# Kernel optimization log

Hardware: AMD Instinct MI355X
Metric: run time of the kernel (lower is better)

The kernel has to match this reference:

```python
import jax, jax.numpy as jnp
import numpy as np

TOP_K = 8
N_EXPERTS = 64
ALPHA = 0.1
NORM_TOPK = True
SEQ_AUX = True


def setup_inputs() -> dict:
    key = jax.random.key(0)
    k1, k2 = jax.random.split(key)
    B, S, H = 4, 4096, 2048
    hidden_states = jax.random.normal(k1, (B, S, H), dtype=jnp.float32)
    # kaiming_uniform_(a=sqrt(5)) => bound = 1/sqrt(fan_in)
    bound = 1.0 / np.sqrt(H)
    weight = jax.random.uniform(k2, (N_EXPERTS, H), dtype=jnp.float32,
                                minval=-bound, maxval=bound)
    return {"hidden_states": hidden_states, "weight": weight}


def reference(hidden_states, weight):
    B, S, H = hidden_states.shape
    E, K = N_EXPERTS, TOP_K
    x = hidden_states.reshape(-1, H)                 # [T, H], T = B*S
    logits = jnp.einsum('th,eh->te', x, weight)      # gating GEMM
    scores = jax.nn.softmax(logits, axis=-1)         # [T, E]
    topk_weight, topk_idx = jax.lax.top_k(scores, K) # [T, K]
    if K > 1 and NORM_TOPK:
        topk_weight = topk_weight / (topk_weight.sum(-1, keepdims=True) + 1e-20)

    # batch-level load stats (bincount over selections)
    expert_loads = jnp.zeros((E,), jnp.float32).at[topk_idx.reshape(-1)].add(1.0)

    # sequence-level auxiliary load-balancing loss
    if SEQ_AUX:
        idx_b = topk_idx.reshape(B, S * K)           # [B, S*K]
        ce = jnp.zeros((B, E), jnp.float32)
        ce = ce.at[jnp.arange(B)[:, None], idx_b].add(1.0)
        ce = ce / (S * K / E)
        mean_scores = scores.reshape(B, S, E).mean(axis=1)   # [B, E]
        aux_loss = (ce * mean_scores).sum(axis=1).mean() * ALPHA
    else:
        ce = jax.nn.one_hot(topk_idx.reshape(-1), E).mean(0)
        Pi = scores.mean(0)
        aux_loss = (Pi * ce * E).sum() * ALPHA

    return (topk_idx, topk_weight, aux_loss, expert_loads)
```

## Files before the change

### kernel.cpp

```cpp
#include <hip/hip_runtime.h>
#include <hip/hip_bf16.h>
#include <math.h>

#define TOK 16384
#define HDIM 2048
#define NE 64
#define NB 4
#define KTOP 8
#define KC 64
#define NC (HDIM / KC)
#define BT 32

typedef __attribute__((ext_vector_type(8))) __bf16 bf16x8;
typedef __attribute__((ext_vector_type(4))) float f32x4;
typedef unsigned int uint;

__device__ __forceinline__ uint asu(float f) { union { float f; uint u; } c; c.f = f; return c.u; }
__device__ __forceinline__ float asf(uint u) { union { uint u; float f; } c; c.u = u; return c.f; }

__device__ __forceinline__ void split3(float v, uint& h, uint& m, uint& l) {
  uint u = asu(v);
  h = u & 0xffff0000u;
  float d = v - asf(h);
  m = asu(d) & 0xffff0000u;
  float d2 = d - asf(m);
  l = asu(d2);
}

__device__ __forceinline__ void split8(float4 a, float4 b,
                                       bf16x8& h8, bf16x8& m8, bf16x8& l8) {
  union { uint4 u; bf16x8 v; } H, M, L;
  uint h0, m0, l0, h1, m1, l1;
  split3(a.x, h0, m0, l0); split3(a.y, h1, m1, l1);
  H.u.x = (h0 >> 16) | (h1 & 0xffff0000u);
  M.u.x = (m0 >> 16) | (m1 & 0xffff0000u);
  L.u.x = (l0 >> 16) | (l1 & 0xffff0000u);
  split3(a.z, h0, m0, l0); split3(a.w, h1, m1, l1);
  H.u.y = (h0 >> 16) | (h1 & 0xffff0000u);
  M.u.y = (m0 >> 16) | (m1 & 0xffff0000u);
  L.u.y = (l0 >> 16) | (l1 & 0xffff0000u);
  split3(b.x, h0, m0, l0); split3(b.y, h1, m1, l1);
  H.u.z = (h0 >> 16) | (h1 & 0xffff0000u);
  M.u.z = (m0 >> 16) | (m1 & 0xffff0000u);
  L.u.z = (l0 >> 16) | (l1 & 0xffff0000u);
  split3(b.z, h0, m0, l0); split3(b.w, h1, m1, l1);
  H.u.w = (h0 >> 16) | (h1 & 0xffff0000u);
  M.u.w = (m0 >> 16) | (m1 & 0xffff0000u);
  L.u.w = (l0 >> 16) | (l1 & 0xffff0000u);
  h8 = H.v; m8 = M.v; l8 = L.v;
}

__device__ __forceinline__ void gl_lds16(const void* g, void* l) {
  __builtin_amdgcn_global_load_lds(
      (const __attribute__((address_space(1))) void*)g,
      (__attribute__((address_space(3))) void*)l, 16, 0, 0);
}

__global__ __launch_bounds__(256) void wsplit(const float* __restrict__ w,
                                              char* __restrict__ wpk,
                                              float* __restrict__ stats) {
  if (blockIdx.x == 0 && threadIdx.x < 128) {
    *(float4*)(stats + threadIdx.x * 4) = make_float4(0.f, 0.f, 0.f, 0.f);
  }
  int t = blockIdx.x * 256 + threadIdx.x;
  int lane = t & 63;
  int f2 = (t >> 6) & 1, half = (t >> 7) & 1, ks = (t >> 8) & 1, c = t >> 9;
  int e = half * 32 + f2 * 16 + (lane & 15);
  int k = c * 64 + ks * 32 + ((lane >> 4) << 3);
  const float* p = w + (size_t)e * HDIM + k;
  bf16x8 h8, m8, l8;
  split8(*(const float4*)p, *(const float4*)(p + 4), h8, m8, l8);
  union { bf16x8 v; uint4 u; } H, M, L;
  H.v = h8; M.v = m8; L.v = l8;
  size_t base = (size_t)c * 24576 + (size_t)ks * 12288 + (size_t)half * 6144
              + (size_t)f2 * 3072 + (size_t)lane * 16;
  *(uint4*)(wpk + base) = H.u;
  *(uint4*)(wpk + base + 1024) = M.u;
  *(uint4*)(wpk + base + 2048) = L.u;
}

__global__ __launch_bounds__(256, 2) void gate_fused(const float* __restrict__ x,
                                                     const char* __restrict__ wpk,
                                                     float* __restrict__ out,
                                                     float* __restrict__ ce,
                                                     float* __restrict__ ssum) {
  __shared__ __align__(16) char lds[65536];
  __shared__ float hist[NE];

  const int tid = threadIdx.x;
  const int bid = blockIdx.x;
  const int t0 = bid * BT;
  const int b = bid >> 7;
  const int lane = tid & 63;
  const int wid = tid >> 6;
  const int half = wid & 1;
  const int tg = (wid >> 1);

  if (tid < NE) hist[tid] = 0.f;

  const char* xsg[2];
  int xdo_[2];
#pragma unroll
  for (int r = 0; r < 2; ++r) {
    int s = r * 256 + tid;
    int stg = s >> 8, sks = (s >> 7) & 1, sq = (s >> 6) & 1, ln = s & 63;
    xsg[r] = (const char*)(x + (size_t)(t0 + stg * 16 + (ln & 15)) * HDIM
                           + sks * 32 + ((ln >> 4) << 3) + sq * 4);
    xdo_[r] = (r * 256 + wid * 64) * 16;
  }
  const char* wsrc = wpk + (size_t)lane * 16;

  f32x4 acc[2] = {{0.f, 0.f, 0.f, 0.f}, {0.f, 0.f, 0.f, 0.f}};

#define STAGE(cc, sel)                                                        \
  {                                                                           \
    char* wdst = lds + (sel) * 24576;                                         \
    const char* wp_ = wsrc + (size_t)(cc) * 24576;                            \
    _Pragma("unroll")                                                         \
    for (int i = 0; i < 6; ++i)                                               \
      gl_lds16(wp_ + (i * 4 + wid) * 1024, wdst + (i * 4 + wid) * 1024);      \
    char* xdst = lds + 49152 + (sel) * 8192;                                  \
    _Pragma("unroll")                                                         \
    for (int r = 0; r < 2; ++r)                                               \
      gl_lds16(xsg[r] + (size_t)(cc) * 256, xdst + xdo_[r]);                  \
  }

  STAGE(0, 0);
  asm volatile("s_waitcnt vmcnt(0)" ::: "memory");
  __builtin_amdgcn_s_barrier();
  asm volatile("" ::: "memory");

#pragma unroll 1
  for (int c = 0; c < NC; ++c) {
    const int sel = c & 1;
    if (c + 1 < NC) STAGE(c + 1, sel ^ 1);

    char* wb = lds + sel * 24576;
    char* xb = lds + 49152 + sel * 8192 + tg * 4096;
#pragma unroll
    for (int ks = 0; ks < 2; ++ks) {
      float4 X0 = *(const float4*)(xb + ks * 2048 + lane * 16);
      float4 X1 = *(const float4*)(xb + ks * 2048 + 1024 + lane * 16);
      bf16x8 ah, am, al;
      split8(X0, X1, ah, am, al);
      const char* wk = wb + ks * 12288 + half * 6144 + lane * 16;
#pragma unroll
      for (int f2 = 0; f2 < 2; ++f2) {
        const char* bb = wk + f2 * 3072;
        bf16x8 bh = *(const bf16x8*)(bb);
        bf16x8 bm = *(const bf16x8*)(bb + 1024);
        bf16x8 bl = *(const bf16x8*)(bb + 2048);
        acc[f2] = __builtin_amdgcn_mfma_f32_16x16x32_bf16(ah, bh, acc[f2], 0, 0, 0);
        acc[f2] = __builtin_amdgcn_mfma_f32_16x16x32_bf16(ah, bm, acc[f2], 0, 0, 0);
        acc[f2] = __builtin_amdgcn_mfma_f32_16x16x32_bf16(am, bh, acc[f2], 0, 0, 0);
        acc[f2] = __builtin_amdgcn_mfma_f32_16x16x32_bf16(ah, bl, acc[f2], 0, 0, 0);
        acc[f2] = __builtin_amdgcn_mfma_f32_16x16x32_bf16(al, bh, acc[f2], 0, 0, 0);
        acc[f2] = __builtin_amdgcn_mfma_f32_16x16x32_bf16(am, bm, acc[f2], 0, 0, 0);
      }
    }
    asm volatile("s_waitcnt vmcnt(0)" ::: "memory");
    __builtin_amdgcn_s_barrier();
    asm volatile("" ::: "memory");
  }
#undef STAGE

  float (*sc)[BT + 1] = (float(*)[BT + 1])lds;
#pragma unroll
  for (int f2 = 0; f2 < 2; ++f2) {
    int e = half * 32 + f2 * 16 + (lane & 15);
    int tk = tg * 16 + ((lane >> 4) << 2);
    sc[e][tk + 0] = acc[f2][0];
    sc[e][tk + 1] = acc[f2][1];
    sc[e][tk + 2] = acc[f2][2];
    sc[e][tk + 3] = acc[f2][3];
  }
  __syncthreads();

  const int t = tid >> 3;
  const int j = tid & 7;
  float p[8];
#pragma unroll
  for (int i = 0; i < 8; ++i) p[i] = sc[j * 8 + i][t];

  float m = p[0];
#pragma unroll
  for (int i = 1; i < 8; ++i) m = fmaxf(m, p[i]);
  m = fmaxf(m, __shfl_xor(m, 1, 8));
  m = fmaxf(m, __shfl_xor(m, 2, 8));
  m = fmaxf(m, __shfl_xor(m, 4, 8));
  float s = 0.f;
#pragma unroll
  for (int i = 0; i < 8; ++i) { p[i] = __expf(p[i] - m); s += p[i]; }
  s += __shfl_xor(s, 1, 8);
  s += __shfl_xor(s, 2, 8);
  s += __shfl_xor(s, 4, 8);
  float inv = 1.f / s;
#pragma unroll
  for (int i = 0; i < 8; ++i) { p[i] *= inv; sc[j * 8 + i][t] = p[i]; }

  unsigned used = 0;
  float wsum = 0.f;
  float wv[KTOP];
  int wi_[KTOP];
#pragma unroll
  for (int sel = 0; sel < KTOP; ++sel) {
    float bv = -1.f;
    int bi = 0;
#pragma unroll
    for (int i = 0; i < 8; ++i) {
      bool ok = !((used >> i) & 1u);
      if (ok && p[i] > bv) { bv = p[i]; bi = i; }
    }
    int ge = j * 8 + bi;
#pragma unroll
    for (int mk = 1; mk < 8; mk <<= 1) {
      float ov = __shfl_xor(bv, mk, 8);
      int og = __shfl_xor(ge, mk, 8);
      if (ov > bv || (ov == bv && og < ge)) { bv = ov; ge = og; }
    }
    if ((ge >> 3) == j) used |= 1u << (ge & 7);
    wv[sel] = bv;
    wi_[sel] = ge;
    wsum += bv;
  }
  if (j == 0) {
    float winv = 1.f / (wsum + 1e-20f);
#pragma unroll
    for (int sel = 0; sel < KTOP; ++sel) {
      out[(size_t)(t0 + t) * KTOP + sel] = (float)wi_[sel];
      out[(size_t)TOK * KTOP + (size_t)(t0 + t) * KTOP + sel] = wv[sel] * winv;
      atomicAdd(&hist[wi_[sel]], 1.f);
    }
  }
  __syncthreads();

  if (tid < NE) {
    float ssl = 0.f;
#pragma unroll
    for (int tt = 0; tt < BT; ++tt) ssl += sc[tid][tt];
    atomicAdd(&ssum[b * NE + tid], ssl);
    atomicAdd(&ce[b * NE + tid], hist[tid]);
  }
}

__global__ __launch_bounds__(64) void gate_final(const float* __restrict__ ce,
                                                 const float* __restrict__ ssum,
                                                 float* __restrict__ out) {
  const int e = threadIdx.x;
  float loads = 0.f, aux = 0.f;
#pragma unroll
  for (int b = 0; b < NB; ++b) {
    float c = ce[b * 64 + e];
    loads += c;
    aux += (c / 512.0f) * (ssum[b * 64 + e] / 4096.0f);
  }
  out[(size_t)2 * TOK * KTOP + 1 + e] = loads;
#pragma unroll
  for (int off = 32; off > 0; off >>= 1) aux += __shfl_down(aux, off);
  if (e == 0) out[(size_t)2 * TOK * KTOP] = aux * (0.1f / 4.0f);
}

extern "C" void kernel_launch(void* const* d_in, const int* in_sizes, int n_in,
                              void* d_out, int out_size, void* d_ws, size_t ws_size,
                              hipStream_t stream) {
  const float* x = (const float*)d_in[0];
  const float* w = (const float*)d_in[1];
  float* out = (float*)d_out;

  char* wpk = (char*)d_ws;
  float* ce = (float*)(wpk + (size_t)NC * 24576);
  float* ssum = ce + NB * NE;

  wsplit<<<dim3(64), dim3(256), 0, stream>>>(w, wpk, ce);
  gate_fused<<<dim3(TOK / BT), dim3(256), 0, stream>>>(x, wpk, out, ce, ssum);
  gate_final<<<dim3(1), dim3(64), 0, stream>>>(ce, ssum, out);
}
```

Measured before the change: 59.00 us.

## Split-K gating GEMM with register-resident weights and separate softmax/top-k kernel

Replaces the single fused kernel with a split-K design. Each block owns one 256-wide K slice, keeps its weight fragments in registers, and streams 256 tokens of x through a triple-buffered LDS pipeline, writing per-slice partial logits to workspace. A second kernel sums the 8 partials, then does softmax, top-k and the stats, and uses a last-block counter to fold in the final aux-loss kernel. The aim is to stop reloading all of W through LDS for every 32-token tile, at the cost of a 32 MB partial-logit round trip through memory and a dependence on workspace size, with the old path kept as a fallback.

Result: slower. 95.81 us (+62.4%).

```diff
diff --git a/kernel.cpp b/kernel.cpp
--- a/kernel.cpp
+++ b/kernel.cpp
@@ -9,7 +9,11 @@
 #define KTOP 8
 #define KC 64
 #define NC (HDIM / KC)
-#define BT 32
+#define NSL 8
+#define TT 256
+#define XCH 16
+#define NXC (TT / XCH)
+#define BTF 32
 
 typedef __attribute__((ext_vector_type(8))) __bf16 bf16x8;
 typedef __attribute__((ext_vector_type(4))) float f32x4;
@@ -59,7 +63,7 @@
 __global__ __launch_bounds__(256) void wsplit(const float* __restrict__ w,
                                               char* __restrict__ wpk,
                                               float* __restrict__ stats) {
-  if (blockIdx.x == 0 && threadIdx.x < 128) {
+  if (blockIdx.x == 0 && threadIdx.x < 132) {
     *(float4*)(stats + threadIdx.x * 4) = make_float4(0.f, 0.f, 0.f, 0.f);
   }
   int t = blockIdx.x * 256 + threadIdx.x;
@@ -79,17 +83,229 @@
   *(uint4*)(wpk + base + 2048) = L.u;
 }
 
-__global__ __launch_bounds__(256, 2) void gate_fused(const float* __restrict__ x,
-                                                     const char* __restrict__ wpk,
-                                                     float* __restrict__ out,
-                                                     float* __restrict__ ce,
-                                                     float* __restrict__ ssum) {
+__global__ __launch_bounds__(512, 4) void gate_k1(const float* __restrict__ x,
+                                                  const char* __restrict__ wpk,
+                                                  float* __restrict__ part) {
+  __shared__ __align__(16) char xlds[3 * 16384];
+  __shared__ float scq[4][XCH][68];
+
+  const int tid = threadIdx.x;
+  const int bid = blockIdx.x;
+  const int slice = bid & 7;
+  const int tile = bid >> 3;
+  const int t0 = tile * TT;
+  const int k0 = slice * 256;
+  const int lane = tid & 63;
+  const int wid = tid >> 6;
+  const int eh = wid & 1;
+  const int kq = wid >> 1;
+
+  bf16x8 Wf[2][2][3];
+  {
+    const char* wb = wpk + (size_t)(slice * 4 + kq) * 24576 + eh * 6144
+                   + (size_t)lane * 16;
+#pragma unroll
+    for (int ks = 0; ks < 2; ++ks)
+#pragma unroll
+      for (int f2 = 0; f2 < 2; ++f2)
+#pragma unroll
+        for (int pl = 0; pl < 3; ++pl)
+          Wf[ks][f2][pl] = *(const bf16x8*)(wb + ks * 12288 + f2 * 3072 + pl * 1024);
+  }
+
+  const char* xsg[2];
+  int xdo_[2];
+#pragma unroll
+  for (int r = 0; r < 2; ++r) {
+    int s = r * 512 + tid;
+    int sks = s >> 7, sq = (s >> 6) & 1, ln = s & 63;
+    xsg[r] = (const char*)(x + (size_t)(t0 + (ln & 15)) * HDIM + k0
+                           + sks * 32 + ((ln >> 4) << 3) + sq * 4);
+    xdo_[r] = (r * 512 + wid * 64) * 16;
+  }
+
+#define STAGE(cc)                                                          \
+  {                                                                        \
+    char* xd = xlds + ((cc) % 3) * 16384;                                  \
+    _Pragma("unroll")                                                      \
+    for (int r = 0; r < 2; ++r)                                            \
+      gl_lds16(xsg[r] + (size_t)(cc) * (XCH * HDIM * 4), xd + xdo_[r]);    \
+  }
+
+  STAGE(0);
+  STAGE(1);
+
+#pragma unroll 1
+  for (int cc = 0; cc < NXC; ++cc) {
+    if (cc + 2 < NXC) STAGE(cc + 2);
+    if (cc + 2 < NXC)      { asm volatile("s_waitcnt vmcnt(4)" ::: "memory"); }
+    else if (cc + 1 < NXC) { asm volatile("s_waitcnt vmcnt(2)" ::: "memory"); }
+    else                   { asm volatile("s_waitcnt vmcnt(0)" ::: "memory"); }
+    __builtin_amdgcn_s_barrier();
+    asm volatile("" ::: "memory");
+
+    f32x4 acc[2] = {{0.f, 0.f, 0.f, 0.f}, {0.f, 0.f, 0.f, 0.f}};
+    const char* xb = xlds + (cc % 3) * 16384;
+#pragma unroll
+    for (int ks = 0; ks < 2; ++ks) {
+      const char* xk = xb + (kq * 2 + ks) * 2048;
+      float4 X0 = *(const float4*)(xk + lane * 16);
+      float4 X1 = *(const float4*)(xk + 1024 + lane * 16);
+      bf16x8 ah, am, al;
+      split8(X0, X1, ah, am, al);
+#pragma unroll
+      for (int f2 = 0; f2 < 2; ++f2) {
+        acc[f2] = __builtin_amdgcn_mfma_f32_16x16x32_bf16(ah, Wf[ks][f2][0], acc[f2], 0, 0, 0);
+        acc[f2] = __builtin_amdgcn_mfma_f32_16x16x32_bf16(ah, Wf[ks][f2][1], acc[f2], 0, 0, 0);
+        acc[f2] = __builtin_amdgcn_mfma_f32_16x16x32_bf16(am, Wf[ks][f2][0], acc[f2], 0, 0, 0);
+        acc[f2] = __builtin_amdgcn_mfma_f32_16x16x32_bf16(ah, Wf[ks][f2][2], acc[f2], 0, 0, 0);
+        acc[f2] = __builtin_amdgcn_mfma_f32_16x16x32_bf16(al, Wf[ks][f2][0], acc[f2], 0, 0, 0);
+        acc[f2] = __builtin_amdgcn_mfma_f32_16x16x32_bf16(am, Wf[ks][f2][1], acc[f2], 0, 0, 0);
+      }
+    }
+#pragma unroll
+    for (int f2 = 0; f2 < 2; ++f2) {
+      int e = eh * 32 + f2 * 16 + (lane & 15);
+      int tk = (lane >> 4) << 2;
+#pragma unroll
+      for (int r = 0; r < 4; ++r)
+        scq[kq][tk + r][e] = acc[f2][r];
+    }
+    __builtin_amdgcn_s_barrier();
+    asm volatile("" ::: "memory");
+    if (wid < 4) {
+#pragma unroll
+      for (int i = 0; i < 4; ++i) {
+        int t = wid * 4 + i;
+        float v = scq[0][t][lane] + scq[1][t][lane]
+                + scq[2][t][lane] + scq[3][t][lane];
+        part[(size_t)(t0 + cc * XCH + t) * (NSL * NE) + slice * NE + lane] = v;
+      }
+    }
+  }
+#undef STAGE
+}
+
+__global__ __launch_bounds__(512) void gate_k2(const float* __restrict__ part,
+                                               float* __restrict__ out,
+                                               float* __restrict__ ce,
+                                               float* __restrict__ ssum,
+                                               int* __restrict__ cnt) {
+  __shared__ float sc[NE][65];
+  __shared__ float hist[NE];
+  __shared__ int lastflag;
+
+  const int tid = threadIdx.x;
+  const int bid = blockIdx.x;
+  const int t0 = bid * 64;
+  const int b = bid >> 6;
+  if (tid < NE) hist[tid] = 0.f;
+
+  const int t = tid >> 3;
+  const int j = tid & 7;
+  float p[8] = {0.f, 0.f, 0.f, 0.f, 0.f, 0.f, 0.f, 0.f};
+  const float* pb = part + (size_t)(t0 + t) * (NSL * NE) + j * 8;
+#pragma unroll
+  for (int s = 0; s < NSL; ++s) {
+    float4 a = *(const float4*)(pb + s * NE);
+    float4 bq = *(const float4*)(pb + s * NE + 4);
+    p[0] += a.x;  p[1] += a.y;  p[2] += a.z;  p[3] += a.w;
+    p[4] += bq.x; p[5] += bq.y; p[6] += bq.z; p[7] += bq.w;
+  }
+
+  float m = p[0];
+#pragma unroll
+  for (int i = 1; i < 8; ++i) m = fmaxf(m, p[i]);
+  m = fmaxf(m, __shfl_xor(m, 1, 8));
+  m = fmaxf(m, __shfl_xor(m, 2, 8));
+  m = fmaxf(m, __shfl_xor(m, 4, 8));
+  float s = 0.f;
+#pragma unroll
+  for (int i = 0; i < 8; ++i) { p[i] = __expf(p[i] - m); s += p[i]; }
+  s += __shfl_xor(s, 1, 8);
+  s += __shfl_xor(s, 2, 8);
+  s += __shfl_xor(s, 4, 8);
+  float inv = 1.f / s;
+#pragma unroll
+  for (int i = 0; i < 8; ++i) { p[i] *= inv; sc[j * 8 + i][t] = p[i]; }
+  __syncthreads();
+
+  unsigned used = 0;
+  float wsum = 0.f;
+  float wv[KTOP];
+  int wi_[KTOP];
+#pragma unroll
+  for (int sel = 0; sel < KTOP; ++sel) {
+    float bv = -1.f;
+    int bi = 0;
+#pragma unroll
+    for (int i = 0; i < 8; ++i) {
+      bool ok = !((used >> i) & 1u);
+      if (ok && p[i] > bv) { bv = p[i]; bi = i; }
+    }
+    int ge = j * 8 + bi;
+#pragma unroll
+    for (int mk = 1; mk < 8; mk <<= 1) {
+      float ov = __shfl_xor(bv, mk, 8);
+      int og = __shfl_xor(ge, mk, 8);
+      if (ov > bv || (ov == bv && og < ge)) { bv = ov; ge = og; }
+    }
+    if ((ge >> 3) == j) used |= 1u << (ge & 7);
+    wv[sel] = bv;
+    wi_[sel] = ge;
+    wsum += bv;
+  }
+  if (j == 0) {
+    float winv = 1.f / (wsum + 1e-20f);
+#pragma unroll
+    for (int sel = 0; sel < KTOP; ++sel) {
+      out[(size_t)(t0 + t) * KTOP + sel] = (float)wi_[sel];
+      out[(size_t)TOK * KTOP + (size_t)(t0 + t) * KTOP + sel] = wv[sel] * winv;
+      atomicAdd(&hist[wi_[sel]], 1.f);
+    }
+  }
+  __syncthreads();
+
+  if (tid < NE) {
+    float ssl = 0.f;
+#pragma unroll
+    for (int tt = 0; tt < 64; ++tt) ssl += sc[tid][tt];
+    atomicAdd(&ssum[b * NE + tid], ssl);
+    atomicAdd(&ce[b * NE + tid], hist[tid]);
+  }
+
+  __threadfence();
+  __syncthreads();
+  if (tid == 0) lastflag = (atomicAdd(cnt, 1) == (int)gridDim.x - 1);
+  __syncthreads();
+  if (lastflag && tid < 64) {
+    const int e = tid;
+    float loads = 0.f, aux = 0.f;
+#pragma unroll
+    for (int b2 = 0; b2 < NB; ++b2) {
+      float cv = atomicAdd(&ce[b2 * 64 + e], 0.f);
+      float sv = atomicAdd(&ssum[b2 * 64 + e], 0.f);
+      loads += cv;
+      aux += (cv / 512.0f) * (sv / 4096.0f);
+    }
+    out[(size_t)2 * TOK * KTOP + 1 + e] = loads;
+#pragma unroll
+    for (int off = 32; off > 0; off >>= 1) aux += __shfl_down(aux, off);
+    if (e == 0) out[(size_t)2 * TOK * KTOP] = aux * (0.1f / 4.0f);
+  }
+}
+
+__global__ __launch_bounds__(256, 2) void gate_fused_fb(const float* __restrict__ x,
+                                                        const char* __restrict__ wpk,
+                                                        float* __restrict__ out,
+                                                        float* __restrict__ ce,
+                                                        float* __restrict__ ssum) {
   __shared__ __align__(16) char lds[65536];
   __shared__ float hist[NE];
 
   const int tid = threadIdx.x;
   const int bid = blockIdx.x;
-  const int t0 = bid * BT;
+  const int t0 = bid * BTF;
   const int b = bid >> 7;
   const int lane = tid & 63;
   const int wid = tid >> 6;
@@ -109,23 +325,22 @@
     xdo_[r] = (r * 256 + wid * 64) * 16;
   }
   const char* wsrc = wpk + (size_t)lane * 16;
-
   f32x4 acc[2] = {{0.f, 0.f, 0.f, 0.f}, {0.f, 0.f, 0.f, 0.f}};
 
-#define STAGE(cc, sel)                                                        \
+#define STAGEF(cc, sel)                                                       \
   {                                                                           \
-    char* wdst = lds + (sel) * 24576;                                         \
     const char* wp_ = wsrc + (size_t)(cc) * 24576;                            \
+    char* wd_ = lds + (sel) * 24576;                                          \
     _Pragma("unroll")                                                         \
     for (int i = 0; i < 6; ++i)                                               \
-      gl_lds16(wp_ + (i * 4 + wid) * 1024, wdst + (i * 4 + wid) * 1024);      \
+      gl_lds16(wp_ + (i * 4 + wid) * 1024, wd_ + (i * 4 + wid) * 1024);       \
     char* xdst = lds + 49152 + (sel) * 8192;                                  \
     _Pragma("unroll")                                                         \
     for (int r = 0; r < 2; ++r)                                               \
       gl_lds16(xsg[r] + (size_t)(cc) * 256, xdst + xdo_[r]);                  \
   }
 
-  STAGE(0, 0);
+  STAGEF(0, 0);
   asm volatile("s_waitcnt vmcnt(0)" ::: "memory");
   __builtin_amdgcn_s_barrier();
   asm volatile("" ::: "memory");
@@ -133,8 +348,7 @@
 #pragma unroll 1
   for (int c = 0; c < NC; ++c) {
     const int sel = c & 1;
-    if (c + 1 < NC) STAGE(c + 1, sel ^ 1);
-
+    if (c + 1 < NC) STAGEF(c + 1, sel ^ 1);
     char* wb = lds + sel * 24576;
     char* xb = lds + 49152 + sel * 8192 + tg * 4096;
 #pragma unroll
@@ -162,9 +376,9 @@
     __builtin_amdgcn_s_barrier();
     asm volatile("" ::: "memory");
   }
-#undef STAGE
-
-  float (*sc)[BT + 1] = (float(*)[BT + 1])lds;
+#undef STAGEF
+
+  float (*sc)[BTF + 1] = (float(*)[BTF + 1])lds;
 #pragma unroll
   for (int f2 = 0; f2 < 2; ++f2) {
     int e = half * 32 + f2 * 16 + (lane & 15);
@@ -181,7 +395,6 @@
   float p[8];
 #pragma unroll
   for (int i = 0; i < 8; ++i) p[i] = sc[j * 8 + i][t];
-
   float m = p[0];
 #pragma unroll
   for (int i = 1; i < 8; ++i) m = fmaxf(m, p[i]);
@@ -233,11 +446,10 @@
     }
   }
   __syncthreads();
-
   if (tid < NE) {
     float ssl = 0.f;
 #pragma unroll
-    for (int tt = 0; tt < BT; ++tt) ssl += sc[tid][tt];
+    for (int tt = 0; tt < BTF; ++tt) ssl += sc[tid][tt];
     atomicAdd(&ssum[b * NE + tid], ssl);
     atomicAdd(&ce[b * NE + tid], hist[tid]);
   }
@@ -268,10 +480,25 @@
   float* out = (float*)d_out;
 
   char* wpk = (char*)d_ws;
-  float* ce = (float*)(wpk + (size_t)NC * 24576);
-  float* ssum = ce + NB * NE;
-
-  wsplit<<<dim3(64), dim3(256), 0, stream>>>(w, wpk, ce);
-  gate_fused<<<dim3(TOK / BT), dim3(256), 0, stream>>>(x, wpk, out, ce, ssum);
-  gate_final<<<dim3(1), dim3(64), 0, stream>>>(ce, ssum, out);
-}
+  const size_t wpk_bytes = (size_t)NC * 24576;
+  const size_t part_elems = (size_t)TOK * NSL * NE;
+  const size_t need = wpk_bytes + part_elems * 4 + 4096;
+
+  if (ws_size >= need) {
+    float* part = (float*)(wpk + wpk_bytes);
+    float* stats = part + part_elems;
+    float* ce = stats;
+    float* ssum = ce + NB * NE;
+    int* cnt = (int*)(ssum + NB * NE);
+    wsplit<<<dim3(64), dim3(256), 0, stream>>>(w, wpk, stats);
+    gate_k1<<<dim3(NSL * (TOK / TT)), dim3(512), 0, stream>>>(x, wpk, part);
+    gate_k2<<<dim3(TOK / 64), dim3(512), 0, stream>>>(part, out, ce, ssum, cnt);
+  } else {
+    float* stats = (float*)(wpk + wpk_bytes);
+    float* ce = stats;
+    float* ssum = ce + NB * NE;
+    wsplit<<<dim3(64), dim3(256), 0, stream>>>(w, wpk, stats);
+    gate_fused_fb<<<dim3(TOK / BTF), dim3(256), 0, stream>>>(x, wpk, out, ce, ssum);
+    gate_final<<<dim3(1), dim3(64), 0, stream>>>(ce, ssum, out);
+  }
+}
```

## Use triple-buffered K=32 stages with two-deep prefetch in gating GEMM

Applied to the files above, without the earlier changes.

The K loop is restructured from double-buffered 64-wide chunks into 32-wide chunks held in a three-slot ring buffer, with loads issued two stages ahead. Partial vmcnt waits let one stage's loads stay in flight across the barrier instead of draining everything each iteration. LDS use drops from 64KB to 48KB per block. In exchange there are twice as many barriers and iterations, each doing half the MFMA work.

New measurement: 72.59 us. 1.23x slower.

```diff
diff --git a/kernel.cpp b/kernel.cpp
--- a/kernel.cpp
+++ b/kernel.cpp
@@ -7,8 +7,8 @@
 #define NE 64
 #define NB 4
 #define KTOP 8
-#define KC 64
-#define NC (HDIM / KC)
+#define NC 32
+#define NC2 64
 #define BT 32
 
 typedef __attribute__((ext_vector_type(8))) __bf16 bf16x8;
@@ -84,7 +84,7 @@
                                                      float* __restrict__ out,
                                                      float* __restrict__ ce,
                                                      float* __restrict__ ssum) {
-  __shared__ __align__(16) char lds[65536];
+  __shared__ __align__(16) char lds[49152];
   __shared__ float hist[NE];
 
   const int tid = threadIdx.x;
@@ -98,67 +98,58 @@
 
   if (tid < NE) hist[tid] = 0.f;
 
-  const char* xsg[2];
-  int xdo_[2];
-#pragma unroll
-  for (int r = 0; r < 2; ++r) {
-    int s = r * 256 + tid;
-    int stg = s >> 8, sks = (s >> 7) & 1, sq = (s >> 6) & 1, ln = s & 63;
-    xsg[r] = (const char*)(x + (size_t)(t0 + stg * 16 + (ln & 15)) * HDIM
-                           + sks * 32 + ((ln >> 4) << 3) + sq * 4);
-    xdo_[r] = (r * 256 + wid * 64) * 16;
-  }
+  const int stg = tid >> 7, sq = (tid >> 6) & 1;
+  const char* xsg = (const char*)(x + (size_t)(t0 + stg * 16 + (lane & 15)) * HDIM
+                                  + ((lane >> 4) << 3) + sq * 4);
+  const int xdo_ = wid * 1024;
   const char* wsrc = wpk + (size_t)lane * 16;
 
   f32x4 acc[2] = {{0.f, 0.f, 0.f, 0.f}, {0.f, 0.f, 0.f, 0.f}};
 
-#define STAGE(cc, sel)                                                        \
+#define STAGE(cc)                                                             \
   {                                                                           \
-    char* wdst = lds + (sel) * 24576;                                         \
-    const char* wp_ = wsrc + (size_t)(cc) * 24576;                            \
+    const char* wp_ = wsrc + (size_t)((cc) >> 1) * 24576 + ((cc) & 1) * 12288; \
+    char* wd_ = lds + ((cc) % 3) * 12288;                                     \
     _Pragma("unroll")                                                         \
-    for (int i = 0; i < 6; ++i)                                               \
-      gl_lds16(wp_ + (i * 4 + wid) * 1024, wdst + (i * 4 + wid) * 1024);      \
-    char* xdst = lds + 49152 + (sel) * 8192;                                  \
-    _Pragma("unroll")                                                         \
-    for (int r = 0; r < 2; ++r)                                               \
-      gl_lds16(xsg[r] + (size_t)(cc) * 256, xdst + xdo_[r]);                  \
-  }
-
-  STAGE(0, 0);
-  asm volatile("s_waitcnt vmcnt(0)" ::: "memory");
+    for (int i = 0; i < 3; ++i)                                               \
+      gl_lds16(wp_ + (i * 4 + wid) * 1024, wd_ + (i * 4 + wid) * 1024);       \
+    gl_lds16(xsg + (size_t)(cc) * 128, lds + 36864 + ((cc) % 3) * 4096 + xdo_); \
+  }
+
+  STAGE(0);
+  STAGE(1);
+  asm volatile("s_waitcnt vmcnt(4)" ::: "memory");
   __builtin_amdgcn_s_barrier();
   asm volatile("" ::: "memory");
 
 #pragma unroll 1
-  for (int c = 0; c < NC; ++c) {
-    const int sel = c & 1;
-    if (c + 1 < NC) STAGE(c + 1, sel ^ 1);
-
-    char* wb = lds + sel * 24576;
-    char* xb = lds + 49152 + sel * 8192 + tg * 4096;
-#pragma unroll
-    for (int ks = 0; ks < 2; ++ks) {
-      float4 X0 = *(const float4*)(xb + ks * 2048 + lane * 16);
-      float4 X1 = *(const float4*)(xb + ks * 2048 + 1024 + lane * 16);
-      bf16x8 ah, am, al;
-      split8(X0, X1, ah, am, al);
-      const char* wk = wb + ks * 12288 + half * 6144 + lane * 16;
-#pragma unroll
-      for (int f2 = 0; f2 < 2; ++f2) {
-        const char* bb = wk + f2 * 3072;
-        bf16x8 bh = *(const bf16x8*)(bb);
-        bf16x8 bm = *(const bf16x8*)(bb + 1024);
-        bf16x8 bl = *(const bf16x8*)(bb + 2048);
-        acc[f2] = __builtin_amdgcn_mfma_f32_16x16x32_bf16(ah, bh, acc[f2], 0, 0, 0);
-        acc[f2] = __builtin_amdgcn_mfma_f32_16x16x32_bf16(ah, bm, acc[f2], 0, 0, 0);
-        acc[f2] = __builtin_amdgcn_mfma_f32_16x16x32_bf16(am, bh, acc[f2], 0, 0, 0);
-        acc[f2] = __builtin_amdgcn_mfma_f32_16x16x32_bf16(ah, bl, acc[f2], 0, 0, 0);
-        acc[f2] = __builtin_amdgcn_mfma_f32_16x16x32_bf16(al, bh, acc[f2], 0, 0, 0);
-        acc[f2] = __builtin_amdgcn_mfma_f32_16x16x32_bf16(am, bm, acc[f2], 0, 0, 0);
-      }
-    }
-    asm volatile("s_waitcnt vmcnt(0)" ::: "memory");
+  for (int c = 0; c < NC2; ++c) {
+    const int sel = c % 3;
+    if (c + 2 < NC2) STAGE(c + 2);
+
+    char* wb = lds + sel * 12288;
+    char* xb = lds + 36864 + sel * 4096 + tg * 2048;
+    float4 X0 = *(const float4*)(xb + lane * 16);
+    float4 X1 = *(const float4*)(xb + 1024 + lane * 16);
+    bf16x8 ah, am, al;
+    split8(X0, X1, ah, am, al);
+    const char* wk = wb + half * 6144 + lane * 16;
+#pragma unroll
+    for (int f2 = 0; f2 < 2; ++f2) {
+      const char* bb = wk + f2 * 3072;
+      bf16x8 bh = *(const bf16x8*)(bb);
+      bf16x8 bm = *(const bf16x8*)(bb + 1024);
+      bf16x8 bl = *(const bf16x8*)(bb + 2048);
+      acc[f2] = __builtin_amdgcn_mfma_f32_16x16x32_bf16(ah, bh, acc[f2], 0, 0, 0);
+      acc[f2] = __builtin_amdgcn_mfma_f32_16x16x32_bf16(ah, bm, acc[f2], 0, 0, 0);
+      acc[f2] = __builtin_amdgcn_mfma_f32_16x16x32_bf16(am, bh, acc[f2], 0, 0, 0);
+      acc[f2] = __builtin_amdgcn_mfma_f32_16x16x32_bf16(ah, bl, acc[f2], 0, 0, 0);
+      acc[f2] = __builtin_amdgcn_mfma_f32_16x16x32_bf16(al, bh, acc[f2], 0, 0, 0);
+      acc[f2] = __builtin_amdgcn_mfma_f32_16x16x32_bf16(am, bm, acc[f2], 0, 0, 0);
+    }
+
+    if (c + 2 < NC2) { asm volatile("s_waitcnt vmcnt(4)" ::: "memory"); }
+    else             { asm volatile("s_waitcnt vmcnt(0)" ::: "memory"); }
     __builtin_amdgcn_s_barrier();
     asm volatile("" ::: "memory");
   }
```
